# Kernel optimization log

Measured on AMD Instinct MI355X. Metric: run time of the kernel, lower is better.

## Reference

```python
import jax, jax.numpy as jnp
import numpy as np

WINDOW = 7
NUM_HEADS = 16
HEAD_DIM = 32  # dim=512 / 16 heads
SCALE = HEAD_DIM ** -0.5


def _relative_position_index(ws: int) -> np.ndarray:
    ch, cw = np.meshgrid(np.arange(ws), np.arange(ws), indexing='ij')
    coords = np.stack([ch, cw]).reshape(2, -1)            # [2, ws*ws]
    rel = coords[:, :, None] - coords[:, None, :]          # [2, N, N]
    rel = rel.transpose(1, 2, 0)                           # [N, N, 2]
    rel[:, :, 0] += ws - 1
    rel[:, :, 1] += ws - 1
    rel[:, :, 0] *= 2 * ws - 1
    return rel.sum(-1)                                     # [N, N]

REL_IDX = jnp.asarray(_relative_position_index(WINDOW))   # [49, 49] int


def setup_inputs() -> dict:
    key = jax.random.key(0)
    ks = jax.random.split(key, 6)
    B, N, C = 2048, WINDOW * WINDOW, NUM_HEADS * HEAD_DIM
    return {
        'hidden_states': jax.random.normal(ks[0], (B, N, C), jnp.float32),
        'attention_mask': jnp.zeros((B, N, N), jnp.float32),
        'qkv_w': jax.random.normal(ks[1], (3 * C, C), jnp.float32) * 0.02,
        'qkv_b': jax.random.normal(ks[2], (3 * C,), jnp.float32) * 0.02,
        'out_w': jax.random.normal(ks[3], (C, C), jnp.float32) * 0.02,
        'out_b': jax.random.normal(ks[4], (C,), jnp.float32) * 0.02,
        'rel_pos_table': jax.random.normal(ks[5], ((2 * WINDOW - 1) ** 2, NUM_HEADS), jnp.float32) * 0.02,
    }


def reference(hidden_states, attention_mask, qkv_w, qkv_b, out_w, out_b, rel_pos_table):
    B, N, C = hidden_states.shape
    H, D = NUM_HEADS, HEAD_DIM
    qkv = hidden_states @ qkv_w.T + qkv_b                  # [B, N, 3C]
    q, k, v = jnp.split(qkv, 3, axis=-1)
    q = q.reshape(B, N, H, D).transpose(0, 2, 1, 3)        # [B, H, N, D]
    k = k.reshape(B, N, H, D).transpose(0, 2, 1, 3)
    v = v.reshape(B, N, H, D).transpose(0, 2, 1, 3)
    attn = jnp.einsum('bhnd,bhmd->bhnm', q, k) * SCALE     # [B, H, N, N]
    # relative position bias: gather [N*N] rows -> [N, N, H] -> [1, H, N, N]
    bias = rel_pos_table[REL_IDX.reshape(-1)].reshape(N, N, H).transpose(2, 0, 1)
    attn = attn + bias[None] + attention_mask[:, None]
    attn = jax.nn.softmax(attn, axis=-1)                   # dropout = identity (eval)
    out = jnp.einsum('bhnm,bhmd->bhnd', attn, v)           # [B, H, N, D]
    out = out.transpose(0, 2, 1, 3).reshape(B, N, C)
    return out @ out_w.T + out_b
```

## Files before the change

### kernel.cpp

```cpp
#include <hip/hip_runtime.h>
#include <hip/hip_bf16.h>

typedef __attribute__((ext_vector_type(8))) __bf16 bf16x8;
typedef __attribute__((ext_vector_type(4))) __bf16 bf16x4;
typedef __attribute__((ext_vector_type(4))) float f32x4;

#define MFMA16(a,b,c) __builtin_amdgcn_mfma_f32_16x16x32_bf16(a,b,c,0,0,0)

__device__ __forceinline__ void gload_lds16(const void* g, void* l) {
  __builtin_amdgcn_global_load_lds(
      (const __attribute__((address_space(1))) void*)g,
      (__attribute__((address_space(3))) void*)l, 16, 0, 0);
}

__device__ __forceinline__ f32x4 max4(f32x4 a, f32x4 b) {
  f32x4 c;
  c[0] = fmaxf(a[0], b[0]); c[1] = fmaxf(a[1], b[1]);
  c[2] = fmaxf(a[2], b[2]); c[3] = fmaxf(a[3], b[3]);
  return c;
}

__global__ void prep_k(const float* __restrict__ qkv_w, const float* __restrict__ out_w,
                       const float* __restrict__ rpt,
                       __bf16* __restrict__ qwb, __bf16* __restrict__ owb,
                       __bf16* __restrict__ biasb)
{
  int i = blockIdx.x * 256 + threadIdx.x;
  if (i < 786432) { qwb[i] = (__bf16)qkv_w[i]; return; }
  i -= 786432;
  if (i < 262144) { owb[i] = (__bf16)out_w[i]; return; }
  i -= 262144;
  if (i < 65536) {
    int hh = i >> 12, qc = i & 4095, qq = qc >> 6, c = qc & 63;
    __bf16 val;
    if (c >= 49)      val = (__bf16)(-30000.0f);
    else if (qq >= 49) val = (__bf16)(0.0f);
    else {
      int dh = qq / 7 - c / 7 + 6;
      int dw = qq % 7 - c % 7 + 6;
      val = (__bf16)rpt[(dh * 13 + dw) * 16 + hh];
    }
    biasb[i] = val;
  }
}

__global__ void cast_k(const float* __restrict__ in, __bf16* __restrict__ outb, int n8)
{
  int i = blockIdx.x * blockDim.x + threadIdx.x;
  int stride = gridDim.x * blockDim.x;
  for (; i < n8; i += stride) {
    const float4* p = (const float4*)in + (size_t)i * 2;
    float4 x = p[0], y = p[1];
    bf16x8 o;
    o[0] = (__bf16)x.x; o[1] = (__bf16)x.y; o[2] = (__bf16)x.z; o[3] = (__bf16)x.w;
    o[4] = (__bf16)y.x; o[5] = (__bf16)y.y; o[6] = (__bf16)y.z; o[7] = (__bf16)y.w;
    ((bf16x8*)outb)[i] = o;
  }
}

template<int EPI>
__global__ __launch_bounds__(256, 2)
void gemm2p(const __bf16* __restrict__ A, const __bf16* __restrict__ Bt,
            const float* __restrict__ bvec, float* __restrict__ outp,
            __bf16* __restrict__ qb, __bf16* __restrict__ kb, __bf16* __restrict__ vb,
            int N, int K)
{
  __shared__ __align__(16) char lds[65536];
  const int tid = threadIdx.x;
  const int wave = tid >> 6, lane = tid & 63;
  const int g = lane >> 4, r = lane & 15;
  const int l8 = lane >> 3, l7 = lane & 7;
  const int wr = wave >> 1, wc = wave & 1;

  const int ntiles = N >> 7;
  const int nper = gridDim.x >> 3;
  const int b2 = (blockIdx.x & 7) * nper + (blockIdx.x >> 3);
  const int m0 = (b2 / ntiles) << 7;
  const int n0 = (b2 % ntiles) << 7;

  const __bf16* Ag = A + (size_t)(m0 + wave * 8 + l8) * K + (l7 ^ l8) * 8;
  const __bf16* Bg = Bt + (size_t)(n0 + wave * 8 + l8) * K + (l7 ^ l8) * 8;
  const size_t r32 = (size_t)32 * K;

  const int ch0 = (g ^ (r & 7)) << 4;
  const int ch1 = ((4 + g) ^ (r & 7)) << 4;
  const char* Arr = lds + (wr * 64 + r) * 128;
  const char* Brr = lds + 16384 + (wc * 64 + r) * 128;

  f32x4 acc[4][4] = {};
  bf16x8 a[4][2], b[4][2];

#pragma unroll
  for (int c = 0; c < 4; ++c) {
    gload_lds16(Ag + c * r32, lds + c * 4096 + wave * 1024);
    gload_lds16(Bg + c * r32, lds + 16384 + c * 4096 + wave * 1024);
  }
#pragma unroll
  for (int c = 0; c < 4; ++c)
    gload_lds16(Ag + 64 + c * r32, lds + 32768 + c * 4096 + wave * 1024);

  const int nkt = K >> 6;
#pragma unroll 1
  for (int kt = 0; kt < nkt; ++kt) {
    const int cur = (kt & 1) << 15;
    if (kt == nkt - 1) asm volatile("s_waitcnt vmcnt(0)" ::: "memory");
    else               asm volatile("s_waitcnt vmcnt(4)" ::: "memory");
    __builtin_amdgcn_s_barrier();

    const char* Ab = Arr + cur;
    const char* Bb = Brr + cur;

#pragma unroll
    for (int mi = 0; mi < 4; ++mi) {
      a[mi][0] = *(const bf16x8*)(Ab + mi * 2048 + ch0);
      a[mi][1] = *(const bf16x8*)(Ab + mi * 2048 + ch1);
    }
#pragma unroll
    for (int ni = 0; ni < 2; ++ni) {
      b[ni][0] = *(const bf16x8*)(Bb + ni * 2048 + ch0);
      b[ni][1] = *(const bf16x8*)(Bb + ni * 2048 + ch1);
    }
    if (kt + 1 < nkt) {
      const __bf16* Bgk = Bg + (kt + 1) * 64;
      char* Bl = lds + (((kt + 1) & 1) << 15) + 16384 + wave * 1024;
#pragma unroll
      for (int c = 0; c < 4; ++c) gload_lds16(Bgk + c * r32, Bl + c * 4096);
    }
    asm volatile("s_waitcnt lgkmcnt(0)" ::: "memory");
    __builtin_amdgcn_s_setprio(1);
#pragma unroll
    for (int mi = 0; mi < 4; ++mi)
#pragma unroll
      for (int ni = 0; ni < 2; ++ni) {
        acc[mi][ni] = MFMA16(a[mi][0], b[ni][0], acc[mi][ni]);
        acc[mi][ni] = MFMA16(a[mi][1], b[ni][1], acc[mi][ni]);
      }
    __builtin_amdgcn_s_setprio(0);
    __builtin_amdgcn_s_barrier();

#pragma unroll
    for (int ni = 2; ni < 4; ++ni) {
      b[ni][0] = *(const bf16x8*)(Bb + ni * 2048 + ch0);
      b[ni][1] = *(const bf16x8*)(Bb + ni * 2048 + ch1);
    }
    if (kt + 2 < nkt) {
      const __bf16* Agk = Ag + (kt + 2) * 64;
      char* Al = lds + cur + wave * 1024;
#pragma unroll
      for (int c = 0; c < 4; ++c) gload_lds16(Agk + c * r32, Al + c * 4096);
    }
    asm volatile("s_waitcnt lgkmcnt(0)" ::: "memory");
    __builtin_amdgcn_s_setprio(1);
#pragma unroll
    for (int mi = 0; mi < 4; ++mi)
#pragma unroll
      for (int ni = 2; ni < 4; ++ni) {
        acc[mi][ni] = MFMA16(a[mi][0], b[ni][0], acc[mi][ni]);
        acc[mi][ni] = MFMA16(a[mi][1], b[ni][1], acc[mi][ni]);
      }
    __builtin_amdgcn_s_setprio(0);
  }

  if (EPI == 1) {
#pragma unroll
    for (int mi = 0; mi < 4; ++mi) {
      int row = m0 + wr * 64 + mi * 16 + g * 4;
#pragma unroll
      for (int ni = 0; ni < 4; ++ni) {
        int col = n0 + wc * 64 + ni * 16 + r;
        float bv = bvec[col];
#pragma unroll
        for (int j = 0; j < 4; ++j)
          outp[(size_t)(row + j) * N + col] = acc[mi][ni][j] + bv;
      }
    }
  } else {
    __bf16* dst; float scl;
    const int which = n0 >> 9;
    if (which == 0)      { dst = qb; scl = 0.17677669529663687f; }
    else if (which == 1) { dst = kb; scl = 1.0f; }
    else                 { dst = vb; scl = 1.0f; }
#pragma unroll
    for (int mi = 0; mi < 4; ++mi) {
#pragma unroll
      for (int ni = 0; ni < 4; ++ni) {
        int n = n0 + wc * 64 + ni * 16 + r;
        float bv = bvec[n];
        int nl = n & 511;
        int hh = nl >> 5, d = nl & 31;
#pragma unroll
        for (int j = 0; j < 4; ++j) {
          int m = m0 + wr * 64 + mi * 16 + g * 4 + j;
          int bb = m / 49, t = m - bb * 49;
          float val = (acc[mi][ni][j] + bv) * scl;
          dst[(((size_t)bb * 16 + hh) * 49 + t) * 32 + d] = (__bf16)val;
        }
      }
    }
  }
}

__global__ __launch_bounds__(256, 4)
void attn_k(const __bf16* __restrict__ qb, const __bf16* __restrict__ kb,
            const __bf16* __restrict__ vb, const __bf16* __restrict__ bias_p,
            const float* __restrict__ mask, __bf16* __restrict__ ao)
{
  __shared__ float maskl[64 * 64];
  __shared__ __bf16 Vt[4][32 * 64];
  __shared__ __bf16 Pl[4][16 * 64];
  const int tid = threadIdx.x, wave = tid >> 6, lane = tid & 63;
  const int g = lane >> 4, r = lane & 15;
  const int b = blockIdx.x >> 2, hg = blockIdx.x & 3;
  const int h = hg * 4 + wave;
  const size_t bh = (size_t)b * 16 + h;
  const __bf16* q = qb + bh * 1568;
  const __bf16* k = kb + bh * 1568;
  const __bf16* v = vb + bh * 1568;
  const bf16x8 z8 = {};
  const f32x4 z4 = {};

  bf16x8* vtz = (bf16x8*)Vt[wave];
#pragma unroll
  for (int i = 0; i < 4; ++i) vtz[i * 64 + lane] = z8;

  const float* mb = mask + (size_t)b * 2401;
#pragma unroll
  for (int i = 0; i < 16; ++i) {
    int idx = i * 256 + tid;
    int qq = idx >> 6, c = idx & 63;
    float mv = (qq < 49 && c < 49) ? mb[qq * 49 + c] : 0.0f;
    maskl[qq * 64 + (c ^ ((qq & 7) << 2))] = mv;
  }

  bf16x8 kf[4], qf[4];
#pragma unroll
  for (int i = 0; i < 4; ++i) {
    int row = i * 16 + r;
    kf[i] = (row < 49) ? *(const bf16x8*)(k + row * 32 + g * 8) : z8;
    qf[i] = (row < 49) ? *(const bf16x8*)(q + row * 32 + g * 8) : z8;
  }

  __syncthreads();

  char* vt = (char*)Vt[wave];
#pragma unroll
  for (int i = 0; i < 4; ++i) {
    int idx = i * 64 + lane;
    int t = idx >> 2, d0 = (idx & 3) << 3;
    if (t < 49) {
      bf16x8 vv = *(const bf16x8*)(v + t * 32 + d0);
#pragma unroll
      for (int j = 0; j < 8; ++j) {
        int d = d0 + j;
        *(__bf16*)(vt + d * 128 + ((t * 2) ^ ((d & 7) << 4))) = vv[j];
      }
    }
  }

  bf16x8 vf[2][2];
#pragma unroll
  for (int di = 0; di < 2; ++di) {
    int row = di * 16 + r;
#pragma unroll
    for (int t = 0; t < 2; ++t)
      vf[di][t] = *(const bf16x8*)(vt + row * 128 + (((t * 32 + g * 8) * 2) ^ ((row & 7) << 4)));
  }

  const __bf16* bp = bias_p + h * 4096;
  char* pw = (char*)Pl[wave];
  __bf16* aob = ao + (size_t)b * 25088 + h * 32;
  const int swz = (r & 7) << 4;
  const int mswz = (r & 7) << 2;

#pragma unroll
  for (int qi = 0; qi < 4; ++qi) {
    f32x4 s[4];
#pragma unroll
    for (int mi = 0; mi < 4; ++mi) s[mi] = MFMA16(kf[mi], qf[qi], z4);

    const int qrow = qi * 16 + r;
#pragma unroll
    for (int mi = 0; mi < 4; ++mi) {
      int c0 = mi * 16 + g * 4;
      bf16x4 b4 = *(const bf16x4*)(bp + qrow * 64 + c0);
      f32x4 m4 = *(const f32x4*)(maskl + qrow * 64 + (c0 ^ mswz));
#pragma unroll
      for (int jj = 0; jj < 4; ++jj)
        s[mi][jj] += (float)b4[jj] + m4[jj];
    }
    f32x4 aa = max4(max4(s[0], s[1]), max4(s[2], s[3]));
    float mx = fmaxf(fmaxf(aa[0], aa[1]), fmaxf(aa[2], aa[3]));
    mx = fmaxf(mx, __shfl_xor(mx, 16));
    mx = fmaxf(mx, __shfl_xor(mx, 32));
    float sum = 0.0f;
#pragma unroll
    for (int mi = 0; mi < 4; ++mi) {
#pragma unroll
      for (int jj = 0; jj < 4; ++jj) {
        float e = __expf(s[mi][jj] - mx);
        s[mi][jj] = e;
        sum += e;
      }
    }
    sum += __shfl_xor(sum, 16);
    sum += __shfl_xor(sum, 32);
    const float rinv = 1.0f / sum;

#pragma unroll
    for (int mi = 0; mi < 4; ++mi) {
      bf16x4 w;
#pragma unroll
      for (int jj = 0; jj < 4; ++jj) w[jj] = (__bf16)(s[mi][jj] * rinv);
      *(bf16x4*)(pw + r * 128 + (((mi * 16 + g * 4) * 2) ^ swz)) = w;
    }
    bf16x8 pa0 = *(const bf16x8*)(pw + r * 128 + ((g * 16) ^ swz));
    bf16x8 pa1 = *(const bf16x8*)(pw + r * 128 + ((64 + g * 16) ^ swz));

#pragma unroll
    for (int di = 0; di < 2; ++di) {
      f32x4 o = MFMA16(pa0, vf[di][0], z4);
      o = MFMA16(pa1, vf[di][1], o);
#pragma unroll
      for (int jj = 0; jj < 4; ++jj) {
        int qq = qi * 16 + g * 4 + jj;
        if (qq < 49)
          aob[(size_t)qq * 512 + di * 16 + r] = (__bf16)o[jj];
      }
    }
  }
}

extern "C" void kernel_launch(void* const* d_in, const int* in_sizes, int n_in,
                              void* d_out, int out_size, void* d_ws, size_t ws_size,
                              hipStream_t stream)
{
  const float* hs    = (const float*)d_in[0];
  const float* mask  = (const float*)d_in[1];
  const float* qkv_w = (const float*)d_in[2];
  const float* qkv_b = (const float*)d_in[3];
  const float* out_w = (const float*)d_in[4];
  const float* out_b = (const float*)d_in[5];
  const float* rpt   = (const float*)d_in[6];
  float* out = (float*)d_out;

  char* ws = (char*)d_ws;
  __bf16* hsb  = (__bf16*)(ws);
  __bf16* qb   = (__bf16*)(ws + 102760448);
  __bf16* kb   = (__bf16*)(ws + 205520896);
  __bf16* vb   = (__bf16*)(ws + 308281344);
  __bf16* qwb  = (__bf16*)(ws + 411041792);
  __bf16* owb  = (__bf16*)(ws + 412614656);
  __bf16* biasb= (__bf16*)(ws + 413138944);

  prep_k<<<4352, 256, 0, stream>>>(qkv_w, out_w, rpt, qwb, owb, biasb);
  cast_k<<<2048, 256, 0, stream>>>(hs, hsb, 6422528);
  gemm2p<0><<<9408, 256, 0, stream>>>(hsb, qwb, qkv_b, nullptr, qb, kb, vb,
                                      1536, 512);
  attn_k<<<8192, 256, 0, stream>>>(qb, kb, vb, biasb, mask, hsb);
  gemm2p<1><<<3136, 256, 0, stream>>>(hsb, owb, out_b, out, nullptr, nullptr, nullptr,
                                      512, 512);
}
```

Baseline: 535.8 us.

## Restructure GEMM main loop into register double-buffered pipeline with vectorized epilogue

Rewrites the GEMM k-loop to stage whole A and B tiles two steps ahead and to prefetch LDS fragments for the next half-step into a second register set while MFMAs run on the current set. Swapping MFMA operand order makes the accumulator layout row-per-lane, so the epilogue can store 4 contiguous values per lane (f32x4 or bf16x4) with vectorized bias loads instead of scalar scattered stores. The aim is to hide LDS latency and cut store instruction count. It raises register pressure, and a full vmcnt(0) wait every iteration may limit how much global-load latency is overlapped.

```diff
diff --git a/kernel.cpp b/kernel.cpp
--- a/kernel.cpp
+++ b/kernel.cpp
@@ -60,7 +60,7 @@
 
 template<int EPI>
 __global__ __launch_bounds__(256, 2)
-void gemm2p(const __bf16* __restrict__ A, const __bf16* __restrict__ Bt,
+void gemmrp(const __bf16* __restrict__ A, const __bf16* __restrict__ Bt,
             const float* __restrict__ bvec, float* __restrict__ outp,
             __bf16* __restrict__ qb, __bf16* __restrict__ kb, __bf16* __restrict__ vb,
             int N, int K)
@@ -81,97 +81,83 @@
   const __bf16* Ag = A + (size_t)(m0 + wave * 8 + l8) * K + (l7 ^ l8) * 8;
   const __bf16* Bg = Bt + (size_t)(n0 + wave * 8 + l8) * K + (l7 ^ l8) * 8;
   const size_t r32 = (size_t)32 * K;
+  char* Ald = lds + wave * 1024 + l8 * 128 + l7 * 16;
 
   const int ch0 = (g ^ (r & 7)) << 4;
   const int ch1 = ((4 + g) ^ (r & 7)) << 4;
-  const char* Arr = lds + (wr * 64 + r) * 128;
-  const char* Brr = lds + 16384 + (wc * 64 + r) * 128;
+  const int arow = (wr * 64 + r) * 128;
+  const int brow = 16384 + (wc * 64 + r) * 128;
 
   f32x4 acc[4][4] = {};
-  bf16x8 a[4][2], b[4][2];
-
-#pragma unroll
-  for (int c = 0; c < 4; ++c) {
-    gload_lds16(Ag + c * r32, lds + c * 4096 + wave * 1024);
-    gload_lds16(Bg + c * r32, lds + 16384 + c * 4096 + wave * 1024);
-  }
-#pragma unroll
-  for (int c = 0; c < 4; ++c)
-    gload_lds16(Ag + 64 + c * r32, lds + 32768 + c * 4096 + wave * 1024);
+  bf16x8 a0[4], b0[4], a1[4], b1[4];
+
+#define STAGE_TILE(T)                                                          \
+  {                                                                            \
+    const __bf16* As_ = Ag + (T) * 64;                                         \
+    const __bf16* Bs_ = Bg + (T) * 64;                                         \
+    char* Ld_ = lds + (((T) & 1) << 15);                                       \
+    _Pragma("unroll")                                                          \
+    for (int c = 0; c < 4; ++c) gload_lds16(As_ + c * r32, Ld_ + (Ald - lds) + c * 4096); \
+    _Pragma("unroll")                                                          \
+    for (int c = 0; c < 4; ++c) gload_lds16(Bs_ + c * r32, Ld_ + (Ald - lds) + 16384 + c * 4096); \
+  }
+
+#define READ_SET(AV, BV, T, CH)                                                \
+  {                                                                            \
+    const char* L_ = lds + (((T) & 1) << 15);                                  \
+    _Pragma("unroll")                                                          \
+    for (int mi = 0; mi < 4; ++mi) AV[mi] = *(const bf16x8*)(L_ + arow + mi * 2048 + (CH)); \
+    _Pragma("unroll")                                                          \
+    for (int ni = 0; ni < 4; ++ni) BV[ni] = *(const bf16x8*)(L_ + brow + ni * 2048 + (CH)); \
+  }
+
+#define MFMA_SET(AV, BV)                                                       \
+  __builtin_amdgcn_s_setprio(1);                                               \
+  _Pragma("unroll")                                                            \
+  for (int mi = 0; mi < 4; ++mi)                                               \
+    _Pragma("unroll")                                                          \
+    for (int ni = 0; ni < 4; ++ni)                                             \
+      acc[mi][ni] = MFMA16(BV[ni], AV[mi], acc[mi][ni]);                       \
+  __builtin_amdgcn_s_setprio(0);
+
+  STAGE_TILE(0);
+  STAGE_TILE(1);
+  asm volatile("s_waitcnt vmcnt(8)" ::: "memory");
+  __builtin_amdgcn_s_barrier();
+  READ_SET(a0, b0, 0, ch0);
+  READ_SET(a1, b1, 0, ch1);
+  asm volatile("s_waitcnt lgkmcnt(8)" ::: "memory");
 
   const int nkt = K >> 6;
 #pragma unroll 1
   for (int kt = 0; kt < nkt; ++kt) {
-    const int cur = (kt & 1) << 15;
-    if (kt == nkt - 1) asm volatile("s_waitcnt vmcnt(0)" ::: "memory");
-    else               asm volatile("s_waitcnt vmcnt(4)" ::: "memory");
+    MFMA_SET(a0, b0);
+    asm volatile("s_waitcnt lgkmcnt(0)" ::: "memory");
+    asm volatile("s_waitcnt vmcnt(0)" ::: "memory");
     __builtin_amdgcn_s_barrier();
-
-    const char* Ab = Arr + cur;
-    const char* Bb = Brr + cur;
-
-#pragma unroll
-    for (int mi = 0; mi < 4; ++mi) {
-      a[mi][0] = *(const bf16x8*)(Ab + mi * 2048 + ch0);
-      a[mi][1] = *(const bf16x8*)(Ab + mi * 2048 + ch1);
-    }
-#pragma unroll
-    for (int ni = 0; ni < 2; ++ni) {
-      b[ni][0] = *(const bf16x8*)(Bb + ni * 2048 + ch0);
-      b[ni][1] = *(const bf16x8*)(Bb + ni * 2048 + ch1);
-    }
+    if (kt + 2 < nkt) STAGE_TILE(kt + 2);
+    if (kt + 1 < nkt) READ_SET(a0, b0, kt + 1, ch0);
+    MFMA_SET(a1, b1);
     if (kt + 1 < nkt) {
-      const __bf16* Bgk = Bg + (kt + 1) * 64;
-      char* Bl = lds + (((kt + 1) & 1) << 15) + 16384 + wave * 1024;
-#pragma unroll
-      for (int c = 0; c < 4; ++c) gload_lds16(Bgk + c * r32, Bl + c * 4096);
-    }
-    asm volatile("s_waitcnt lgkmcnt(0)" ::: "memory");
-    __builtin_amdgcn_s_setprio(1);
-#pragma unroll
-    for (int mi = 0; mi < 4; ++mi)
-#pragma unroll
-      for (int ni = 0; ni < 2; ++ni) {
-        acc[mi][ni] = MFMA16(a[mi][0], b[ni][0], acc[mi][ni]);
-        acc[mi][ni] = MFMA16(a[mi][1], b[ni][1], acc[mi][ni]);
-      }
-    __builtin_amdgcn_s_setprio(0);
-    __builtin_amdgcn_s_barrier();
-
-#pragma unroll
-    for (int ni = 2; ni < 4; ++ni) {
-      b[ni][0] = *(const bf16x8*)(Bb + ni * 2048 + ch0);
-      b[ni][1] = *(const bf16x8*)(Bb + ni * 2048 + ch1);
-    }
-    if (kt + 2 < nkt) {
-      const __bf16* Agk = Ag + (kt + 2) * 64;
-      char* Al = lds + cur + wave * 1024;
-#pragma unroll
-      for (int c = 0; c < 4; ++c) gload_lds16(Agk + c * r32, Al + c * 4096);
-    }
-    asm volatile("s_waitcnt lgkmcnt(0)" ::: "memory");
-    __builtin_amdgcn_s_setprio(1);
-#pragma unroll
-    for (int mi = 0; mi < 4; ++mi)
-#pragma unroll
-      for (int ni = 2; ni < 4; ++ni) {
-        acc[mi][ni] = MFMA16(a[mi][0], b[ni][0], acc[mi][ni]);
-        acc[mi][ni] = MFMA16(a[mi][1], b[ni][1], acc[mi][ni]);
-      }
-    __builtin_amdgcn_s_setprio(0);
-  }
+      READ_SET(a1, b1, kt + 1, ch1);
+      asm volatile("s_waitcnt lgkmcnt(8)" ::: "memory");
+    }
+  }
+
+  f32x4 bv4[4];
+#pragma unroll
+  for (int ni = 0; ni < 4; ++ni)
+    bv4[ni] = *(const f32x4*)(bvec + n0 + wc * 64 + ni * 16 + g * 4);
 
   if (EPI == 1) {
 #pragma unroll
     for (int mi = 0; mi < 4; ++mi) {
-      int row = m0 + wr * 64 + mi * 16 + g * 4;
+      int row = m0 + wr * 64 + mi * 16 + r;
+      float* orow = outp + (size_t)row * N + n0 + wc * 64 + g * 4;
 #pragma unroll
       for (int ni = 0; ni < 4; ++ni) {
-        int col = n0 + wc * 64 + ni * 16 + r;
-        float bv = bvec[col];
-#pragma unroll
-        for (int j = 0; j < 4; ++j)
-          outp[(size_t)(row + j) * N + col] = acc[mi][ni][j] + bv;
+        f32x4 w = acc[mi][ni] + bv4[ni];
+        *(f32x4*)(orow + ni * 16) = w;
       }
     }
   } else {
@@ -180,24 +166,31 @@
     if (which == 0)      { dst = qb; scl = 0.17677669529663687f; }
     else if (which == 1) { dst = kb; scl = 1.0f; }
     else                 { dst = vb; scl = 1.0f; }
-#pragma unroll
-    for (int mi = 0; mi < 4; ++mi) {
+    int hh_[4], d0_[4];
+#pragma unroll
+    for (int ni = 0; ni < 4; ++ni) {
+      int nl = (n0 + wc * 64 + ni * 16) & 511;
+      hh_[ni] = nl >> 5;
+      d0_[ni] = (nl & 31) + g * 4;
+    }
+#pragma unroll
+    for (int mi = 0; mi < 4; ++mi) {
+      int m = m0 + wr * 64 + mi * 16 + r;
+      int bb = m / 49, t = m - bb * 49;
+      __bf16* dr = dst + (size_t)bb * 25088 + t * 32;
 #pragma unroll
       for (int ni = 0; ni < 4; ++ni) {
-        int n = n0 + wc * 64 + ni * 16 + r;
-        float bv = bvec[n];
-        int nl = n & 511;
-        int hh = nl >> 5, d = nl & 31;
-#pragma unroll
-        for (int j = 0; j < 4; ++j) {
-          int m = m0 + wr * 64 + mi * 16 + g * 4 + j;
-          int bb = m / 49, t = m - bb * 49;
-          float val = (acc[mi][ni][j] + bv) * scl;
-          dst[(((size_t)bb * 16 + hh) * 49 + t) * 32 + d] = (__bf16)val;
-        }
-      }
-    }
-  }
+        f32x4 v = acc[mi][ni];
+        bf16x4 w;
+#pragma unroll
+        for (int j = 0; j < 4; ++j) w[j] = (__bf16)((v[j] + bv4[ni][j]) * scl);
+        *(bf16x4*)(dr + hh_[ni] * 1568 + d0_[ni]) = w;
+      }
+    }
+  }
+#undef STAGE_TILE
+#undef READ_SET
+#undef MFMA_SET
 }
 
 __global__ __launch_bounds__(256, 4)
@@ -354,9 +347,9 @@
 
   prep_k<<<4352, 256, 0, stream>>>(qkv_w, out_w, rpt, qwb, owb, biasb);
   cast_k<<<2048, 256, 0, stream>>>(hs, hsb, 6422528);
-  gemm2p<0><<<9408, 256, 0, stream>>>(hsb, qwb, qkv_b, nullptr, qb, kb, vb,
+  gemmrp<0><<<9408, 256, 0, stream>>>(hsb, qwb, qkv_b, nullptr, qb, kb, vb,
                                       1536, 512);
   attn_k<<<8192, 256, 0, stream>>>(qb, kb, vb, biasb, mask, hsb);
-  gemm2p<1><<<3136, 256, 0, stream>>>(hsb, owb, out_b, out, nullptr, nullptr, nullptr,
+  gemmrp<1><<<3136, 256, 0, stream>>>(hsb, owb, out_b, out, nullptr, nullptr, nullptr,
                                       512, 512);
 }
```

After: 553.7 us. +3.4%, slower.
